# Kernel optimization log

Hardware: AMD Instinct MI355X
Metric: run time of the kernel (lower is better)

## Reference

```python
import jax, jax.numpy as jnp
import numpy as np
import math

EMBED_DIM = 1024
NUM_HEADS = 16
B, T = 4, 2048
HEAD_DIM = EMBED_DIM // NUM_HEADS


def setup_inputs() -> dict:
    key = jax.random.key(0)
    ks = jax.random.split(key, 9)
    s = 1.0 / math.sqrt(EMBED_DIM)
    x = jax.random.normal(ks[0], (B, T, EMBED_DIM), dtype=jnp.float32)
    # causal mask, broadcastable over (B, H)
    mask = jnp.tril(jnp.ones((T, T), dtype=bool))[None, None, :, :]
    Wq = jax.random.normal(ks[1], (EMBED_DIM, EMBED_DIM), dtype=jnp.float32) * s
    bq = jnp.zeros((EMBED_DIM,), dtype=jnp.float32)
    Wk = jax.random.normal(ks[2], (EMBED_DIM, EMBED_DIM), dtype=jnp.float32) * s
    bk = jnp.zeros((EMBED_DIM,), dtype=jnp.float32)
    Wv = jax.random.normal(ks[3], (EMBED_DIM, EMBED_DIM), dtype=jnp.float32) * s
    bv = jnp.zeros((EMBED_DIM,), dtype=jnp.float32)
    Wo = jax.random.normal(ks[4], (EMBED_DIM, EMBED_DIM), dtype=jnp.float32) * s
    bo = jnp.zeros((EMBED_DIM,), dtype=jnp.float32)
    return {"x": x, "mask": mask, "Wq": Wq, "bq": bq, "Wk": Wk, "bk": bk,
            "Wv": Wv, "bv": bv, "Wo": Wo, "bo": bo}


def reference(x, mask, Wq, bq, Wk, bk, Wv, bv, Wo, bo):
    Bsz, Tlen, C = x.shape
    H, D = NUM_HEADS, HEAD_DIM
    q = (x @ Wq + bq).reshape(Bsz, Tlen, H, D).transpose(0, 2, 1, 3)  # [B,H,T,D]
    k = (x @ Wk + bk).reshape(Bsz, Tlen, H, D).transpose(0, 2, 1, 3)
    v = (x @ Wv + bv).reshape(Bsz, Tlen, H, D).transpose(0, 2, 1, 3)
    scores = jnp.einsum('bhtd,bhsd->bhts', q, k) / math.sqrt(D)  # [B,H,T,T]
    scores = jnp.where(mask, scores, jnp.float32(-1e9))
    attn = jax.nn.softmax(scores, axis=-1)
    out = jnp.einsum('bhts,bhsd->bhtd', attn, v)  # [B,H,T,D]
    out = out.transpose(0, 2, 1, 3).reshape(Bsz, Tlen, C)
    return out @ Wo + bo
```

## Files before the change

kernel.cpp:

```cpp
#include <hip/hip_runtime.h>

#define SEQ   2048
#define NH    16
#define HD    64
#define EMB   1024
#define NB    4
#define MTOT  (NB*SEQ)
#define NT    (SEQ/64)

typedef _Float16 f16;
typedef _Float16 f16x4 __attribute__((ext_vector_type(4)));
typedef _Float16 f16x8 __attribute__((ext_vector_type(8)));
typedef float    f32x4 __attribute__((ext_vector_type(4)));

#define MFMA_F16(a,b,c) __builtin_amdgcn_mfma_f32_16x16x32_f16(a,b,c,0,0,0)

#define QSCALE 0.18033688011112043f

__device__ __forceinline__ void gload16(const f16* g, f16* l) {
  __builtin_amdgcn_global_load_lds(
      (const __attribute__((address_space(1))) void*)g,
      (__attribute__((address_space(3))) void*)l, 16, 0, 0);
}

__global__ __launch_bounds__(256) void cast_x_kernel(
    const float* __restrict__ x, f16* __restrict__ xh) {
  size_t i = ((size_t)blockIdx.x * 256 + threadIdx.x) * 8;
  float4 a = *(const float4*)(x + i);
  float4 b = *(const float4*)(x + i + 4);
  f16x8 o;
  o[0]=(f16)a.x; o[1]=(f16)a.y; o[2]=(f16)a.z; o[3]=(f16)a.w;
  o[4]=(f16)b.x; o[5]=(f16)b.y; o[6]=(f16)b.z; o[7]=(f16)b.w;
  *(f16x8*)(xh + i) = o;
}

__global__ __launch_bounds__(256) void wtrans_kernel(
    const float* __restrict__ W0, const float* __restrict__ W1,
    const float* __restrict__ W2, const float* __restrict__ W3,
    f16* __restrict__ O0, f16* __restrict__ O1,
    f16* __restrict__ O2, f16* __restrict__ O3) {
  const int z = blockIdx.z;
  const float* W = (z==0)?W0:(z==1)?W1:(z==2)?W2:W3;
  f16* O        = (z==0)?O0:(z==1)?O1:(z==2)?O2:O3;
  __shared__ float Tl[64][68];
  const int t = threadIdx.x;
  const int k0 = blockIdx.x * 64, n0 = blockIdx.y * 64;
  {
    const int r = t >> 2, c0 = (t & 3) * 16;
    const float* src = W + (size_t)(k0 + r) * EMB + n0 + c0;
    #pragma unroll
    for (int j = 0; j < 4; ++j) {
      float4 v = *(const float4*)(src + 4 * j);
      Tl[c0+4*j+0][r]=v.x; Tl[c0+4*j+1][r]=v.y;
      Tl[c0+4*j+2][r]=v.z; Tl[c0+4*j+3][r]=v.w;
    }
  }
  __syncthreads();
  {
    const int n = t >> 2, c0 = (t & 3) * 16;
    f16* dst = O + (size_t)(n0 + n) * EMB + k0 + c0;
    #pragma unroll
    for (int j = 0; j < 2; ++j) {
      f16x8 o;
      #pragma unroll
      for (int u = 0; u < 8; ++u) o[u] = (f16)Tl[n][c0 + 8*j + u];
      *(f16x8*)(dst + 8 * j) = o;
    }
  }
}

template<int MODE>
__device__ __forceinline__ void gemm_core(
    const f16* __restrict__ A, const f16* __restrict__ Bt,
    const float* __restrict__ bias, void* __restrict__ out,
    int m0, int n0, float scale) {
  __shared__ f16 As[128 * 64];
  __shared__ f16 Bs[128 * 64];
  const int tid  = threadIdx.x;
  const int lane = tid & 63, w = tid >> 6;
  const int g = lane >> 4, lx = lane & 15;
  const int wr = w >> 1, wc = w & 1;
  const int sr = lane >> 3, sc = lane & 7;

  f32x4 acc[4][4];
  const f32x4 z4 = {0.f, 0.f, 0.f, 0.f};
  #pragma unroll
  for (int i = 0; i < 4; ++i)
    #pragma unroll
    for (int j = 0; j < 4; ++j) acc[i][j] = z4;

  for (int k0 = 0; k0 < EMB; k0 += 64) {
    __syncthreads();
    #pragma unroll
    for (int ci = 0; ci < 4; ++ci) {
      const int i = 4 * w + ci;
      const int r = i * 8 + sr;
      const int c = sc ^ (r & 7);
      gload16(A  + (size_t)(m0 + r) * EMB + k0 + c * 8, &As[i * 512]);
      gload16(Bt + (size_t)(n0 + r) * EMB + k0 + c * 8, &Bs[i * 512]);
    }
    __syncthreads();

    #pragma unroll
    for (int h = 0; h < 2; ++h) {
      f16x8 af[4], bf[4];
      #pragma unroll
      for (int mf = 0; mf < 4; ++mf) {
        const int row = wr * 64 + mf * 16 + lx;
        const int off = (row * 128 + h * 64 + g * 16) ^ ((row & 7) << 4);
        af[mf] = *(const f16x8*)((const char*)As + off);
      }
      #pragma unroll
      for (int nf = 0; nf < 4; ++nf) {
        const int row = wc * 64 + nf * 16 + lx;
        const int off = (row * 128 + h * 64 + g * 16) ^ ((row & 7) << 4);
        bf[nf] = *(const f16x8*)((const char*)Bs + off);
      }
      #pragma unroll
      for (int mf = 0; mf < 4; ++mf)
        #pragma unroll
        for (int nf = 0; nf < 4; ++nf)
          acc[mf][nf] = MFMA_F16(af[mf], bf[nf], acc[mf][nf]);
    }
  }

  #pragma unroll
  for (int mf = 0; mf < 4; ++mf) {
    #pragma unroll
    for (int nf = 0; nf < 4; ++nf) {
      const int n  = n0 + wc * 64 + nf * 16 + lx;
      const int mb = m0 + wr * 64 + mf * 16 + g * 4;
      const float bv = bias[n];
      if (MODE == 2) {
        float* op = (float*)out;
        #pragma unroll
        for (int r = 0; r < 4; ++r)
          op[(size_t)(mb + r) * EMB + n] = acc[mf][nf][r] + bv;
      } else {
        const int b = mb >> 11, tt = mb & (SEQ - 1);
        const int hh = n >> 6, d = n & (HD - 1);
        f16* op = (f16*)out;
        if (MODE == 0) {
          #pragma unroll
          for (int r = 0; r < 4; ++r)
            op[((size_t)(b * NH + hh) * SEQ + tt + r) * HD + d] =
                (f16)((acc[mf][nf][r] + bv) * scale);
        } else {
          f16x4 o;
          #pragma unroll
          for (int r = 0; r < 4; ++r) o[r] = (f16)(acc[mf][nf][r] + bv);
          *(f16x4*)(op + ((size_t)(b * NH + hh) * HD + d) * SEQ + tt) = o;
        }
      }
    }
  }
}

__global__ __launch_bounds__(256) void qk_gemm_kernel(
    const f16* __restrict__ xh, const f16* __restrict__ wqt,
    const f16* __restrict__ wkt, const float* __restrict__ bq,
    const float* __restrict__ bk, f16* __restrict__ qh, f16* __restrict__ kh) {
  const int z = blockIdx.z;
  gemm_core<0>(xh, z ? wkt : wqt, z ? bk : bq, z ? kh : qh,
               blockIdx.x * 128, blockIdx.y * 128, z ? 1.0f : QSCALE);
}

__global__ __launch_bounds__(256) void v_gemm_kernel(
    const f16* __restrict__ xh, const f16* __restrict__ wvt,
    const float* __restrict__ bv, f16* __restrict__ vth) {
  gemm_core<1>(xh, wvt, bv, vth, blockIdx.x * 128, blockIdx.y * 128, 1.0f);
}

__global__ __launch_bounds__(256) void proj_gemm_kernel(
    const f16* __restrict__ ath, const f16* __restrict__ wot,
    const float* __restrict__ bo, float* __restrict__ out) {
  gemm_core<2>(ath, wot, bo, out, blockIdx.x * 128, blockIdx.y * 128, 1.0f);
}

__global__ __launch_bounds__(256, 4) void attn_kernel(
    const f16* __restrict__ Qh, const f16* __restrict__ Kh,
    const f16* __restrict__ Vth, f16* __restrict__ Att) {
  __shared__ f16 Ks[64 * 64];
  __shared__ f16 Vs[64 * 64];
  __shared__ f16 Ps[4][16 * 64];
  const int tid  = threadIdx.x;
  const int lane = tid & 63, w = tid >> 6;
  const int g = lane >> 4, lx = lane & 15;
  const int sr = lane >> 3, sc = lane & 7;
  const int bid = blockIdx.x;
  const int xcd = bid & 7;
  const int idx = bid >> 3;
  const int p   = idx & 15;
  const int bh  = xcd + 8 * (idx >> 4);
  const int qlo = p, qhi = NT - 1 - p;
  const int nkt = qhi + 1;
  const f16* qp = Qh  + (size_t)bh * SEQ * HD;
  const f16* kp = Kh  + (size_t)bh * SEQ * HD;
  const f16* vp = Vth + (size_t)bh * HD * SEQ;
  const int row0[2] = {qlo * 64 + w * 16, qhi * 64 + w * 16};

  f16x8 qf[2][2];
  #pragma unroll
  for (int part = 0; part < 2; ++part) {
    const int qrow = row0[part] + lx;
    #pragma unroll
    for (int h = 0; h < 2; ++h)
      qf[part][h] = *(const f16x8*)(qp + (size_t)qrow * HD + h * 32 + g * 8);
  }

  const f32x4 z4 = {0.f, 0.f, 0.f, 0.f};
  f32x4 oa[2][4];
  float m_i[2] = {-1e30f, -1e30f}, l_i[2] = {0.f, 0.f};
  #pragma unroll
  for (int part = 0; part < 2; ++part)
    #pragma unroll
    for (int df = 0; df < 4; ++df) oa[part][df] = z4;

  for (int kt = 0; kt < nkt; ++kt) {
    __syncthreads();
    #pragma unroll
    for (int ci = 0; ci < 2; ++ci) {
      const int i = 2 * w + ci;
      const int r = i * 8 + sr;
      const int c = sc ^ (r & 7);
      gload16(kp + (size_t)(kt * 64 + r) * HD + c * 8, &Ks[i * 512]);
      gload16(vp + (size_t)r * SEQ + kt * 64 + c * 8,  &Vs[i * 512]);
    }
    __syncthreads();

    const int npart = (kt <= qlo) ? 2 : 1;
    #pragma unroll
    for (int pi = 0; pi < 2; ++pi) {
      if (pi >= npart) continue;
      const int part = 1 - pi;
      const int qrow = row0[part] + lx;
      const bool diag = (kt == (part ? qhi : qlo));

      f32x4 sa[4];
      #pragma unroll
      for (int sf = 0; sf < 4; ++sf) sa[sf] = z4;
      __builtin_amdgcn_s_setprio(1);
      #pragma unroll
      for (int h = 0; h < 2; ++h)
        #pragma unroll
        for (int sf = 0; sf < 4; ++sf) {
          const int row = sf * 16 + lx;
          const int off = (row * 128 + h * 64 + g * 16) ^ ((row & 7) << 4);
          f16x8 kf = *(const f16x8*)((const char*)Ks + off);
          sa[sf] = MFMA_F16(kf, qf[part][h], sa[sf]);
        }
      __builtin_amdgcn_s_setprio(0);

      float rmax = -1e30f;
      #pragma unroll
      for (int sf = 0; sf < 4; ++sf)
        #pragma unroll
        for (int r = 0; r < 4; ++r) {
          float vsc = sa[sf][r];
          if (diag) {
            const int kv = kt * 64 + sf * 16 + g * 4 + r;
            if (kv > qrow) vsc = -1e30f;
          }
          sa[sf][r] = vsc;
          rmax = fmaxf(rmax, vsc);
        }
      rmax = fmaxf(rmax, __shfl_xor(rmax, 16));
      rmax = fmaxf(rmax, __shfl_xor(rmax, 32));
      const float mnew = fmaxf(m_i[part], rmax);
      const float corr = exp2f(m_i[part] - mnew);
      m_i[part] = mnew;
      float rsum = 0.f;
      #pragma unroll
      for (int sf = 0; sf < 4; ++sf)
        #pragma unroll
        for (int r = 0; r < 4; ++r) {
          const float pv = exp2f(sa[sf][r] - mnew);
          sa[sf][r] = pv;
          rsum += pv;
        }
      rsum += __shfl_xor(rsum, 16);
      rsum += __shfl_xor(rsum, 32);
      l_i[part] = l_i[part] * corr + rsum;

      #pragma unroll
      for (int sf = 0; sf < 4; ++sf) {
        f16x4 p4;
        #pragma unroll
        for (int r = 0; r < 4; ++r) p4[r] = (f16)sa[sf][r];
        const int off = (lx * 128 + sf * 32 + g * 8) ^ ((lx & 7) << 4);
        *(f16x4*)((char*)Ps[w] + off) = p4;
      }

      #pragma unroll
      for (int r = 0; r < 4; ++r) {
        const float cr = __shfl(corr, g * 4 + r, 64);
        #pragma unroll
        for (int df = 0; df < 4; ++df) oa[part][df][r] *= cr;
      }

      __builtin_amdgcn_s_setprio(1);
      #pragma unroll
      for (int hk = 0; hk < 2; ++hk) {
        const int offp = (lx * 128 + hk * 64 + g * 16) ^ ((lx & 7) << 4);
        f16x8 pf = *(const f16x8*)((const char*)Ps[w] + offp);
        #pragma unroll
        for (int df = 0; df < 4; ++df) {
          const int row = df * 16 + lx;
          const int offv = (row * 128 + hk * 64 + g * 16) ^ ((row & 7) << 4);
          f16x8 vf = *(const f16x8*)((const char*)Vs + offv);
          oa[part][df] = MFMA_F16(pf, vf, oa[part][df]);
        }
      }
      __builtin_amdgcn_s_setprio(0);
    }
  }

  const int b = bh >> 4, hh = bh & 15;
  #pragma unroll
  for (int part = 0; part < 2; ++part) {
    const float inv = 1.f / l_i[part];
    #pragma unroll
    for (int r = 0; r < 4; ++r) {
      const float ir = __shfl(inv, g * 4 + r, 64);
      const int t = row0[part] + g * 4 + r;
      f16* dst = Att + ((size_t)b * SEQ + t) * EMB + hh * HD;
      #pragma unroll
      for (int df = 0; df < 4; ++df)
        dst[df * 16 + lx] = (f16)(oa[part][df][r] * ir);
    }
  }
}

extern "C" void kernel_launch(void* const* d_in, const int* in_sizes, int n_in,
                              void* d_out, int out_size, void* d_ws, size_t ws_size,
                              hipStream_t stream) {
  (void)in_sizes; (void)n_in; (void)out_size; (void)ws_size;
  const float* x  = (const float*)d_in[0];
  const float* Wq = (const float*)d_in[2];
  const float* bq = (const float*)d_in[3];
  const float* Wk = (const float*)d_in[4];
  const float* bk = (const float*)d_in[5];
  const float* Wv = (const float*)d_in[6];
  const float* bv = (const float*)d_in[7];
  const float* Wo = (const float*)d_in[8];
  const float* bo = (const float*)d_in[9];

  f16* xh  = (f16*)d_ws;
  f16* wqt = xh  + (size_t)MTOT * EMB;
  f16* wkt = wqt + (size_t)EMB * EMB;
  f16* wvt = wkt + (size_t)EMB * EMB;
  f16* wot = wvt + (size_t)EMB * EMB;
  f16* qh  = wot + (size_t)EMB * EMB;
  f16* kh  = qh  + (size_t)MTOT * EMB;
  f16* vth = kh  + (size_t)MTOT * EMB;
  f16* ath = vth + (size_t)MTOT * EMB;

  cast_x_kernel<<<dim3(MTOT * EMB / (256 * 8)), 256, 0, stream>>>(x, xh);
  wtrans_kernel<<<dim3(16, 16, 4), 256, 0, stream>>>(
      Wq, Wk, Wv, Wo, wqt, wkt, wvt, wot);
  qk_gemm_kernel<<<dim3(MTOT / 128, EMB / 128, 2), 256, 0, stream>>>(
      xh, wqt, wkt, bq, bk, qh, kh);
  v_gemm_kernel<<<dim3(MTOT / 128, EMB / 128), 256, 0, stream>>>(
      xh, wvt, bv, vth);
  attn_kernel<<<dim3((NT / 2) * NB * NH), 256, 0, stream>>>(qh, kh, vth, ath);
  proj_gemm_kernel<<<dim3(MTOT / 128, EMB / 128), 256, 0, stream>>>(
      ath, wot, bo, (float*)d_out);
}
```

Baseline: 201.7 us.

## Merge QKV GEMM launches and add lazy softmax rescale with deferred row sums

The separate QK and V projection launches become a single three-slice kernel, which removes one launch and the tail idle time between them. In the attention kernel, the running max is only updated, and the output accumulators rescaled, when some lane's local max exceeds the stored max by more than 8 (a FA4-style conditional rescale). Cross-lane row-sum shuffles move out of the loop and run once at the end, and exp2f is replaced with the hardware exp2 builtin. The risk is fp16 overflow in P when values are not rescaled (bounded by 2^8), plus the new wave-wide vote branch.

```diff
diff --git a/kernel.cpp b/kernel.cpp
--- a/kernel.cpp
+++ b/kernel.cpp
@@ -16,6 +16,14 @@
 #define MFMA_F16(a,b,c) __builtin_amdgcn_mfma_f32_16x16x32_f16(a,b,c,0,0,0)
 
 #define QSCALE 0.18033688011112043f
+
+__device__ __forceinline__ float fast_exp2(float x) {
+#if __has_builtin(__builtin_amdgcn_exp2f)
+  return __builtin_amdgcn_exp2f(x);
+#else
+  return exp2f(x);
+#endif
+}
 
 __device__ __forceinline__ void gload16(const f16* g, f16* l) {
   __builtin_amdgcn_global_load_lds(
@@ -156,19 +164,17 @@
   }
 }
 
-__global__ __launch_bounds__(256) void qk_gemm_kernel(
+__global__ __launch_bounds__(256) void qkv_gemm_kernel(
     const f16* __restrict__ xh, const f16* __restrict__ wqt,
-    const f16* __restrict__ wkt, const float* __restrict__ bq,
-    const float* __restrict__ bk, f16* __restrict__ qh, f16* __restrict__ kh) {
+    const f16* __restrict__ wkt, const f16* __restrict__ wvt,
+    const float* __restrict__ bq, const float* __restrict__ bk,
+    const float* __restrict__ bv,
+    f16* __restrict__ qh, f16* __restrict__ kh, f16* __restrict__ vth) {
   const int z = blockIdx.z;
-  gemm_core<0>(xh, z ? wkt : wqt, z ? bk : bq, z ? kh : qh,
-               blockIdx.x * 128, blockIdx.y * 128, z ? 1.0f : QSCALE);
-}
-
-__global__ __launch_bounds__(256) void v_gemm_kernel(
-    const f16* __restrict__ xh, const f16* __restrict__ wvt,
-    const float* __restrict__ bv, f16* __restrict__ vth) {
-  gemm_core<1>(xh, wvt, bv, vth, blockIdx.x * 128, blockIdx.y * 128, 1.0f);
+  const int m0 = blockIdx.x * 128, n0 = blockIdx.y * 128;
+  if (z == 0)      gemm_core<0>(xh, wqt, bq, qh, m0, n0, QSCALE);
+  else if (z == 1) gemm_core<0>(xh, wkt, bk, kh, m0, n0, 1.0f);
+  else             gemm_core<1>(xh, wvt, bv, vth, m0, n0, 1.0f);
 }
 
 __global__ __launch_bounds__(256) void proj_gemm_kernel(
@@ -251,7 +257,7 @@
         }
       __builtin_amdgcn_s_setprio(0);
 
-      float rmax = -1e30f;
+      float lmax = -1e30f;
       #pragma unroll
       for (int sf = 0; sf < 4; ++sf)
         #pragma unroll
@@ -259,28 +265,37 @@
           float vsc = sa[sf][r];
           if (diag) {
             const int kv = kt * 64 + sf * 16 + g * 4 + r;
-            if (kv > qrow) vsc = -1e30f;
+            if (kv > qrow) { vsc = -1e30f; sa[sf][r] = vsc; }
           }
-          sa[sf][r] = vsc;
-          rmax = fmaxf(rmax, vsc);
-        }
-      rmax = fmaxf(rmax, __shfl_xor(rmax, 16));
-      rmax = fmaxf(rmax, __shfl_xor(rmax, 32));
-      const float mnew = fmaxf(m_i[part], rmax);
-      const float corr = exp2f(m_i[part] - mnew);
-      m_i[part] = mnew;
+          lmax = fmaxf(lmax, vsc);
+        }
+
+      if (!__all(lmax <= m_i[part] + 8.f)) {
+        float rmax = fmaxf(lmax, __shfl_xor(lmax, 16));
+        rmax = fmaxf(rmax, __shfl_xor(rmax, 32));
+        const float mnew = fmaxf(m_i[part], rmax);
+        const float corr = fast_exp2(m_i[part] - mnew);
+        m_i[part] = mnew;
+        l_i[part] *= corr;
+        #pragma unroll
+        for (int r = 0; r < 4; ++r) {
+          const float cr = __shfl(corr, g * 4 + r, 64);
+          #pragma unroll
+          for (int df = 0; df < 4; ++df) oa[part][df][r] *= cr;
+        }
+      }
+
+      const float mcur = m_i[part];
       float rsum = 0.f;
       #pragma unroll
       for (int sf = 0; sf < 4; ++sf)
         #pragma unroll
         for (int r = 0; r < 4; ++r) {
-          const float pv = exp2f(sa[sf][r] - mnew);
+          const float pv = fast_exp2(sa[sf][r] - mcur);
           sa[sf][r] = pv;
           rsum += pv;
         }
-      rsum += __shfl_xor(rsum, 16);
-      rsum += __shfl_xor(rsum, 32);
-      l_i[part] = l_i[part] * corr + rsum;
+      l_i[part] += rsum;
 
       #pragma unroll
       for (int sf = 0; sf < 4; ++sf) {
@@ -289,13 +304,6 @@
         for (int r = 0; r < 4; ++r) p4[r] = (f16)sa[sf][r];
         const int off = (lx * 128 + sf * 32 + g * 8) ^ ((lx & 7) << 4);
         *(f16x4*)((char*)Ps[w] + off) = p4;
-      }
-
-      #pragma unroll
-      for (int r = 0; r < 4; ++r) {
-        const float cr = __shfl(corr, g * 4 + r, 64);
-        #pragma unroll
-        for (int df = 0; df < 4; ++df) oa[part][df][r] *= cr;
       }
 
       __builtin_amdgcn_s_setprio(1);
@@ -318,7 +326,10 @@
   const int b = bh >> 4, hh = bh & 15;
   #pragma unroll
   for (int part = 0; part < 2; ++part) {
-    const float inv = 1.f / l_i[part];
+    float lf = l_i[part];
+    lf += __shfl_xor(lf, 16);
+    lf += __shfl_xor(lf, 32);
+    const float inv = 1.f / lf;
     #pragma unroll
     for (int r = 0; r < 4; ++r) {
       const float ir = __shfl(inv, g * 4 + r, 64);
@@ -358,10 +369,8 @@
   cast_x_kernel<<<dim3(MTOT * EMB / (256 * 8)), 256, 0, stream>>>(x, xh);
   wtrans_kernel<<<dim3(16, 16, 4), 256, 0, stream>>>(
       Wq, Wk, Wv, Wo, wqt, wkt, wvt, wot);
-  qk_gemm_kernel<<<dim3(MTOT / 128, EMB / 128, 2), 256, 0, stream>>>(
-      xh, wqt, wkt, bq, bk, qh, kh);
-  v_gemm_kernel<<<dim3(MTOT / 128, EMB / 128), 256, 0, stream>>>(
-      xh, wvt, bv, vth);
+  qkv_gemm_kernel<<<dim3(MTOT / 128, EMB / 128, 3), 256, 0, stream>>>(
+      xh, wqt, wkt, wvt, bq, bk, bv, qh, kh, vth);
   attn_kernel<<<dim3((NT / 2) * NB * NH), 256, 0, stream>>>(qh, kh, vth, ath);
   proj_gemm_kernel<<<dim3(MTOT / 128, EMB / 128), 256, 0, stream>>>(
       ath, wot, bo, (float*)d_out);
```

Measured after the change: 223.9 us. 1.11x slower.
